# Kernel tuning notes

Hardware: AMD Instinct MI355X
Metric: run time of the kernel (lower is better)

Reference implementation:

```python
import math
import jax, jax.numpy as jnp
import numpy as np

B, P, L = 32, 128, 64
DIN, TE, H, NH, NL = 16, 64, 512, 8, 2
DH = H // NH
DP = DIN + TE
TAU = 300.0
DELTA = 300.0

_PARAM_SPEC = [
    ("te_scale_w", (1, 1)), ("te_scale_b", (1,)),
    ("te_per_w", (TE - 1, 1)), ("te_per_b", (TE - 1,)),
    ("inp_w", (H, DP)), ("inp_b", (H,)),
    ("wq", (H, H)), ("bq", (H,)), ("wk", (H, H)), ("bk", (H,)),
    ("wv", (H, H)), ("bv", (H,)), ("wo", (H, H)), ("bo", (H,)),
    ("ffn_w1", (H, H)), ("ffn_b1", (H,)), ("ffn_w2", (H, H)), ("ffn_b2", (H,)),
    ("ln1_g", (H,)), ("ln1_b", (H,)), ("ln2_g", (H,)), ("ln2_b", (H,)),
    ("exists_bias", (1, 1, H)),
    ("gwq", (NL, H, H)), ("gbq", (NL, H)), ("gwk", (NL, H, H)), ("gbk", (NL, H)),
    ("gwv", (NL, H, H)), ("gbv", (NL, H)), ("gwo", (NL, H, H)), ("gbo", (NL, H)),
]


def setup_inputs() -> dict:
    key = jax.random.key(0)
    ks = jax.random.split(key, 3 + len(_PARAM_SPEC))
    inp = {
        "x": jax.random.normal(ks[0], (B, P, L, DIN), jnp.float32),
        "tt": jax.random.uniform(ks[1], (B, P, L, 1), jnp.float32),
        "mask": jax.random.randint(ks[2], (B, P, L, 1), 0, 2).astype(jnp.int32),
    }
    for i, (name, shp) in enumerate(_PARAM_SPEC):
        inp[name] = 0.02 * jax.random.normal(ks[3 + i], shp, jnp.float32)
    # LayerNorm affine params: gamma=1, beta=0
    inp["ln1_g"] = jnp.ones((H,), jnp.float32)
    inp["ln1_b"] = jnp.zeros((H,), jnp.float32)
    inp["ln2_g"] = jnp.ones((H,), jnp.float32)
    inp["ln2_b"] = jnp.zeros((H,), jnp.float32)
    return inp


def _layernorm(x, g, b, eps=1e-5):
    m = x.mean(-1, keepdims=True)
    v = ((x - m) ** 2).mean(-1, keepdims=True)
    return (x - m) / jnp.sqrt(v + eps) * g + b


def _time_bias(m):
    idx = jnp.arange(m)
    dist = jnp.abs(idx[:, None] - idx[None, :]).astype(jnp.float32) * DELTA
    return jnp.log(jnp.exp(-dist / TAU) + 1e-12)  # [P, P]


def _pos_encoding(p, d):
    pos = jnp.arange(p, dtype=jnp.float32)[:, None]
    div = jnp.exp(jnp.arange(0, d, 2, dtype=jnp.float32) * (-math.log(10000.0) / d))
    pe = jnp.zeros((p, d), jnp.float32)
    pe = pe.at[:, 0::2].set(jnp.sin(pos * div))
    pe = pe.at[:, 1::2].set(jnp.cos(pos * div))
    return pe


def reference(x, tt, mask,
              te_scale_w, te_scale_b, te_per_w, te_per_b,
              inp_w, inp_b, wq, bq, wk, bk, wv, bv, wo, bo,
              ffn_w1, ffn_b1, ffn_w2, ffn_b2, ln1_g, ln1_b, ln2_g, ln2_b,
              exists_bias, gwq, gbq, gwk, gbk, gwv, gbv, gwo, gbo):
    b, p, l, _ = x.shape
    # --- Learnable time embedding: scale linear + sin(periodic linear), concat ---
    te1 = tt @ te_scale_w.T + te_scale_b                      # [B,P,L,1]
    te2 = jnp.sin(tt @ te_per_w.T + te_per_b)                 # [B,P,L,TE-1]
    pts = jnp.concatenate([x, te1, te2], axis=-1)             # [B,P,L,DP]

    valid = (mask[..., 0] > 0).reshape(b * p, l)              # [N,L] bool
    h = (pts.reshape(b * p, l, DP) @ inp_w.T) + inp_b         # [N,L,H]

    has_any = jnp.any(valid, axis=1)                          # [N]
    key_pad = ~valid
    # Empty patches: unmask position 0 and zero its features
    key_pad = key_pad.at[:, 0].set(key_pad[:, 0] & has_any)
    pos0 = (jnp.arange(l) == 0)[None, :, None]
    h = jnp.where((~has_any)[:, None, None] & pos0, 0.0, h)

    # --- Intra-patch MHA (GAT) ---
    def heads(t, w, bias):
        return ((t @ w.T) + bias).reshape(b * p, l, NH, DH)
    q, k, v = heads(h, wq, bq), heads(h, wk, bk), heads(h, wv, bv)
    sc = jnp.einsum("nqhd,nkhd->nhqk", q, k) / math.sqrt(DH)
    sc = jnp.where(key_pad[:, None, None, :], -1e9, sc)
    z = jnp.einsum("nhqk,nkhd->nqhd", jax.nn.softmax(sc, axis=-1), v)
    z = z.reshape(b * p, l, H) @ wo.T + bo
    h = _layernorm(h + z, ln1_g, ln1_b)
    ffn = jax.nn.relu(h @ ffn_w1.T + ffn_b1) @ ffn_w2.T + ffn_b2
    h = _layernorm(h + ffn, ln2_g, ln2_b)

    # Masked mean pooling -> patch tokens
    w = valid.astype(jnp.float32)[..., None]                  # [N,L,1]
    denom = jnp.clip(w.sum(axis=1), 1.0)
    h = ((h * w).sum(axis=1) / denom).reshape(b, p, H)        # [B,P,H]

    # Exists bias for missing patches + positional encoding
    pexists = has_any.reshape(b, p).astype(jnp.float32)       # [B,P]
    h = h + exists_bias * (1.0 - pexists)[..., None]
    h = h + _pos_encoding(p, H)[None]

    # --- Patch-level time-biased graph attention stack (residual) ---
    tb = _time_bias(p)[None, None]                            # [1,1,P,P]
    kp = (pexists <= 0.0)[:, None, None, :]                   # [B,1,1,P]
    for li in range(NL):
        def gh(t, w, bias):
            return ((t @ w.T) + bias).reshape(b, p, NH, DH)
        q = gh(h, gwq[li], gbq[li])
        k = gh(h, gwk[li], gbk[li])
        v = gh(h, gwv[li], gbv[li])
        att = jnp.einsum("bqhd,bkhd->bhqk", q, k) / math.sqrt(DH) + tb
        att = jnp.where(kp, -1e9, att)
        out = jnp.einsum("bhqk,bkhd->bqhd", jax.nn.softmax(att, axis=-1), v)
        out = out.reshape(b, p, H) @ gwo[li].T + gbo[li]
        out = out * pexists[..., None]
        h = h + out
    return h
```

## Files before the change

### kernel.cpp

```cpp
#include <hip/hip_runtime.h>

#define NTOK 4096
#define CH   512
#define NCHUNK 8

typedef _Float16 f16;
typedef __attribute__((ext_vector_type(8))) _Float16 half8;
typedef __attribute__((ext_vector_type(4))) _Float16 half4;
typedef __attribute__((ext_vector_type(4))) float f32x4;

#define OFF_INPW 0
#define OFF_WQKV (512*128)
#define OFF_WO   (OFF_WQKV + 3*512*512)
#define OFF_W1   (OFF_WO + 512*512)
#define OFF_W2   (OFF_W1 + 512*512)
#define OFF_GW   (OFF_W2 + 512*512)
#define WBF_TOT  (OFF_GW + 8*512*512)

static __device__ __forceinline__ f32x4 mfma16(half8 a, half8 b, f32x4 c){
  return __builtin_amdgcn_mfma_f32_16x16x32_f16(a, b, c, 0, 0, 0);
}

static __device__ __forceinline__ void gld_lds16(const f16* g, f16* l){
  __builtin_amdgcn_global_load_lds(
      (const __attribute__((address_space(1))) void*)g,
      (__attribute__((address_space(3))) void*)l, 16, 0, 0);
}

__global__ __launch_bounds__(256) void conv_weights(
    const float* __restrict__ inpw, const float* __restrict__ wq, const float* __restrict__ wk,
    const float* __restrict__ wv, const float* __restrict__ wo, const float* __restrict__ w1,
    const float* __restrict__ w2, const float* __restrict__ gwq, const float* __restrict__ gwk,
    const float* __restrict__ gwv, const float* __restrict__ gwo, f16* __restrict__ wbf,
    const float* __restrict__ bq, const float* __restrict__ bk, const float* __restrict__ bv,
    const float* __restrict__ gbq, const float* __restrict__ gbk, const float* __restrict__ gbv,
    float* __restrict__ biasb)
{
  int e = blockIdx.x*256 + threadIdx.x;
  int y = blockIdx.y;
  if (y == 0){
    if (e < 512*128){
      int row = e>>7, col = e&127;
      float v = (col < 80) ? inpw[row*80 + col] : 0.f;
      wbf[OFF_INPW + e] = (f16)v;
    }
    return;
  }
  if (y == 15){
    if (e < 1536){
      biasb[e] = (e < 512) ? bq[e] : (e < 1024 ? bk[e-512] : bv[e-1024]);
    } else if (e < 3*1536){
      int idx = e - 1536, li = idx/1536, c = idx - li*1536;
      float v = (c < 512) ? gbq[li*512 + c] : (c < 1024 ? gbk[li*512 + c-512] : gbv[li*512 + c-1024]);
      biasb[e] = v;
    }
    return;
  }
  if (e >= 512*512) return;
  const float* src; int off;
  if (y <= 6){
    const float* tab[6] = {wq, wk, wv, wo, w1, w2};
    src = tab[y-1]; off = OFF_WQKV + (y-1)*512*512;
  } else {
    int idx = y-7; int li = idx>>2, part = idx&3;
    const float* tab[4] = {gwq, gwk, gwv, gwo};
    src = tab[part] + (size_t)li*512*512; off = OFF_GW + idx*512*512;
  }
  wbf[off + e] = (f16)src[e];
}

__global__ __launch_bounds__(256) void build_mask(
    const int* __restrict__ mask, float* __restrict__ mb, float* __restrict__ pex)
{
  int wv = threadIdx.x>>6, lane = threadIdx.x&63;
  int n = blockIdx.x*4 + wv;
  int valid = mask[(size_t)n*64 + lane] > 0;
  unsigned long long ball = __ballot(valid);
  int hasany = (ball != 0ull);
  int masked = (lane == 0) ? (!valid && hasany) : (!valid);
  mb[(size_t)n*64 + lane] = masked ? -1e9f : 0.f;
  if (lane == 0) pex[n] = hasany ? 1.f : 0.f;
}

__global__ __launch_bounds__(256) void pts_build(
    const float* __restrict__ x, const float* __restrict__ tt,
    const float* __restrict__ tsw, const float* __restrict__ tsb,
    const float* __restrict__ tpw, const float* __restrict__ tpb,
    f16* __restrict__ pts, int rowbase)
{
  int e = blockIdx.x*256 + threadIdx.x;
  int r = e>>7, col = e&127;
  size_t grow = (size_t)rowbase + r;
  float v;
  if (col < 16) v = x[grow*16 + col];
  else if (col >= 80) v = 0.f;
  else {
    float t = tt[grow];
    if (col == 16) v = t*tsw[0] + tsb[0];
    else           v = __sinf(t*tpw[col-17] + tpb[col-17]);
  }
  pts[e] = (f16)v;
}

template<int RESID, bool RELU, bool OUTF32, bool ZEMPTY>
__global__ __launch_bounds__(256) void gemm128(
    const f16* __restrict__ A, const f16* __restrict__ W, const float* __restrict__ bias,
    void* __restrict__ Cout, const void* __restrict__ Rsd, const float* __restrict__ pex,
    int K, int lda, int ldc, int nbase)
{
  __shared__ __align__(16) f16 As[128][64];
  __shared__ __align__(16) f16 Bs[128][64];
  const int tid = threadIdx.x;
  const int m0 = blockIdx.x*128, n0 = blockIdx.y*128;
  const int wv = tid>>6, lane = tid&63, l15 = lane&15, quad = lane>>4;
  const int wm = (wv&1)*64, wn = (wv>>1)*64;
  const int srow = lane>>3;
  const int schunk = (lane&7) ^ srow;
  f32x4 acc[4][4] = {};
  for (int kc = 0; kc < K; kc += 64){
    __syncthreads();
    #pragma unroll
    for (int i=0; i<4; i++){
      const int rA = wv*32 + i*8;
      gld_lds16(A + (size_t)(m0 + rA + srow)*lda + kc + schunk*8, &As[rA][0]);
      gld_lds16(W + (size_t)(n0 + rA + srow)*K   + kc + schunk*8, &Bs[rA][0]);
    }
    __syncthreads();
    #pragma unroll
    for (int kk=0; kk<2; kk++){
      half8 av[4], bv8[4];
      #pragma unroll
      for (int t=0; t<4; t++){
        const int ra = wm + t*16 + l15;
        av[t]  = *(const half8*)(&As[ra][(((kk*4 + quad) ^ (ra&7)))*8]);
        const int rb = wn + t*16 + l15;
        bv8[t] = *(const half8*)(&Bs[rb][(((kk*4 + quad) ^ (rb&7)))*8]);
      }
      #pragma unroll
      for (int mt=0; mt<4; mt++)
        #pragma unroll
        for (int nt=0; nt<4; nt++)
          acc[mt][nt] = mfma16(av[mt], bv8[nt], acc[mt][nt]);
    }
  }
  #pragma unroll
  for (int mt=0; mt<4; mt++){
    #pragma unroll
    for (int nt=0; nt<4; nt++){
      #pragma unroll
      for (int i=0; i<4; i++){
        int gr = m0 + wm + mt*16 + quad*4 + i;
        int gc = n0 + wn + nt*16 + l15;
        float v = acc[mt][nt][i] + bias[gc];
        if (RELU) v = fmaxf(v, 0.f);
        if (RESID == 1) v += (float)((const f16*)Rsd)[(size_t)gr*ldc + gc];
        if (ZEMPTY){ if ((gr&63)==0 && pex[nbase + (gr>>6)]==0.f) v = 0.f; }
        if (RESID == 2) v = v*pex[gr] + ((const float*)Rsd)[(size_t)gr*ldc + gc];
        if (OUTF32) ((float*)Cout)[(size_t)gr*ldc + gc] = v;
        else        ((f16*)Cout)[(size_t)gr*ldc + gc] = (f16)v;
      }
    }
  }
}

__global__ __launch_bounds__(128) void attn_patch(
    f16* __restrict__ qkv, const float* __restrict__ maskbias, int nbase)
{
  __shared__ f16 Vt[2][64][72];
  __shared__ f16 Ps[2][64][72];
  __shared__ float mbs[64];
  const int tid = threadIdx.x, wv = tid>>6, lane = tid&63, l15 = lane&15, quad = lane>>4;
  const int n = blockIdx.x, h = blockIdx.y*2 + wv;
  if (tid < 64) mbs[tid] = maskbias[(size_t)(nbase+n)*64 + tid];
  const f16* Vb = qkv + 1024 + h*64;
  for (int i=0; i<64; i++)
    Vt[wv][lane][i] = Vb[((size_t)n*64 + i)*1536 + lane];
  __syncthreads();
  const f16* Qb  = qkv + (size_t)n*64*1536 + h*64;
  const f16* Kbb = Qb + 512;
  f32x4 sacc[4][4] = {};
  #pragma unroll
  for (int kc=0; kc<2; kc++){
    half8 af[4], bf[4];
    #pragma unroll
    for (int t4=0; t4<4; t4++){
      af[t4] = *(const half8*)(Qb  + (size_t)(t4*16 + l15)*1536 + kc*32 + quad*8);
      bf[t4] = *(const half8*)(Kbb + (size_t)(t4*16 + l15)*1536 + kc*32 + quad*8);
    }
    #pragma unroll
    for (int ti=0; ti<4; ti++)
      #pragma unroll
      for (int tj=0; tj<4; tj++)
        sacc[ti][tj] = mfma16(af[ti], bf[tj], sacc[ti][tj]);
  }
  #pragma unroll
  for (int ti=0; ti<4; ti++){
    #pragma unroll
    for (int i=0; i<4; i++){
      float mx = -1e30f;
      #pragma unroll
      for (int tj=0; tj<4; tj++){
        float sv = sacc[ti][tj][i]*0.125f + mbs[tj*16 + l15];
        sacc[ti][tj][i] = sv;
        mx = fmaxf(mx, sv);
      }
      #pragma unroll
      for (int off=1; off<16; off<<=1) mx = fmaxf(mx, __shfl_xor(mx, off, 64));
      float sum = 0.f;
      #pragma unroll
      for (int tj=0; tj<4; tj++){
        float pv = __expf(sacc[ti][tj][i] - mx);
        sacc[ti][tj][i] = pv; sum += pv;
      }
      #pragma unroll
      for (int off=1; off<16; off<<=1) sum += __shfl_xor(sum, off, 64);
      float inv = 1.f/sum;
      int q = ti*16 + quad*4 + i;
      #pragma unroll
      for (int tj=0; tj<4; tj++)
        Ps[wv][q][tj*16 + l15] = (f16)(sacc[ti][tj][i]*inv);
    }
  }
  __syncthreads();
  f32x4 zacc[4][4] = {};
  #pragma unroll
  for (int kc=0; kc<2; kc++){
    half8 va[4], pb[4];
    #pragma unroll
    for (int t4=0; t4<4; t4++){
      va[t4] = *(const half8*)(&Vt[wv][t4*16 + l15][kc*32 + quad*8]);
      pb[t4] = *(const half8*)(&Ps[wv][t4*16 + l15][kc*32 + quad*8]);
    }
    #pragma unroll
    for (int ti2=0; ti2<4; ti2++)
      #pragma unroll
      for (int tj=0; tj<4; tj++)
        zacc[ti2][tj] = mfma16(va[ti2], pb[tj], zacc[ti2][tj]);
  }
  __syncthreads();
  #pragma unroll
  for (int ti2=0; ti2<4; ti2++)
    #pragma unroll
    for (int tj=0; tj<4; tj++){
      int q = tj*16 + l15, d0 = ti2*16 + quad*4;
      half4 pk;
      #pragma unroll
      for (int i=0; i<4; i++) pk[i] = (f16)zacc[ti2][tj][i];
      *(half4*)(&Vt[wv][q][d0]) = pk;
    }
  __syncthreads();
  #pragma unroll
  for (int i=0; i<8; i++){
    int q = i*8 + (lane>>3), d0 = (lane&7)*8;
    *(uint4*)(qkv + ((size_t)n*64 + q)*1536 + h*64 + d0) = *(const uint4*)(&Vt[wv][q][d0]);
  }
}

__global__ __launch_bounds__(256) void ln_rows(
    const f16* __restrict__ X, f16* __restrict__ Y,
    const float* __restrict__ g, const float* __restrict__ b)
{
  int wv = threadIdx.x>>6, lane = threadIdx.x&63;
  size_t row = (size_t)blockIdx.x*4 + wv;
  half8 raw = *(const half8*)(X + row*512 + lane*8);
  float xv[8];
  #pragma unroll
  for (int j=0; j<8; j++) xv[j] = (float)raw[j];
  float s = 0.f;
  #pragma unroll
  for (int j=0; j<8; j++) s += xv[j];
  #pragma unroll
  for (int off=1; off<64; off<<=1) s += __shfl_xor(s, off, 64);
  float mean = s*(1.f/512.f);
  float vs = 0.f;
  #pragma unroll
  for (int j=0; j<8; j++){ float d = xv[j]-mean; vs += d*d; }
  #pragma unroll
  for (int off=1; off<64; off<<=1) vs += __shfl_xor(vs, off, 64);
  float rstd = rsqrtf(vs*(1.f/512.f) + 1e-5f);
  half8 o;
  #pragma unroll
  for (int j=0; j<8; j++){
    int c = lane*8 + j;
    o[j] = (f16)((xv[j]-mean)*rstd*g[c] + b[c]);
  }
  *(half8*)(Y + row*512 + lane*8) = o;
}

__global__ __launch_bounds__(256) void pool_ln2(
    const f16* __restrict__ X, const int* __restrict__ mask,
    const float* __restrict__ g, const float* __restrict__ b, const float* __restrict__ eb,
    float* __restrict__ out, int nbase)
{
  __shared__ float mArr[64], rArr[64], vArr[64];
  const int tid = threadIdx.x, wv = tid>>6, lane = tid&63;
  const int n = blockIdx.x, ng = nbase + n, p = ng & 127;
  for (int j=0; j<16; j++){
    int l = wv*16 + j;
    half8 raw = *(const half8*)(X + ((size_t)n*64 + l)*512 + lane*8);
    float s=0.f, ss=0.f;
    #pragma unroll
    for (int jj=0; jj<8; jj++){ float f = (float)raw[jj]; s += f; ss += f*f; }
    #pragma unroll
    for (int off=1; off<64; off<<=1){ s += __shfl_xor(s, off, 64); ss += __shfl_xor(ss, off, 64); }
    if (lane == 0){
      float m = s*(1.f/512.f);
      mArr[l] = m; rArr[l] = rsqrtf(ss*(1.f/512.f) - m*m + 1e-5f);
    }
  }
  if (tid < 64) vArr[tid] = (mask[(size_t)ng*64 + tid] > 0) ? 1.f : 0.f;
  __syncthreads();
  float cnt = 0.f;
  #pragma unroll
  for (int l=0; l<64; l++) cnt += vArr[l];
  float denom = fmaxf(cnt, 1.f);
  float pexv = cnt > 0.f ? 1.f : 0.f;
  float a0=0.f, a1=0.f;
  for (int l=0; l<64; l++){
    float wgt = vArr[l], m = mArr[l], rs = rArr[l];
    float x0 = (float)X[((size_t)n*64+l)*512 + tid];
    float x1 = (float)X[((size_t)n*64+l)*512 + tid + 256];
    a0 += wgt*(x0-m)*rs; a1 += wgt*(x1-m)*rs;
  }
  #pragma unroll
  for (int k=0; k<2; k++){
    int c = tid + k*256;
    float acc = k ? a1 : a0;
    float fr = __expf(-(float)(c & ~1) * (9.210340371976184f/512.f));
    float ang = (float)p * fr;
    float pe = (c & 1) ? cosf(ang) : sinf(ang);
    float o = (g[c]*acc + b[c]*cnt)/denom + eb[c]*(1.f - pexv) + pe;
    out[(size_t)ng*512 + c] = o;
  }
}

__global__ __launch_bounds__(256) void cvt_f32_f16(const float* __restrict__ s, f16* __restrict__ d){
  int i = blockIdx.x*256 + threadIdx.x;
  d[i] = (f16)s[i];
}

__global__ __launch_bounds__(256) void attn_graph(
    f16* __restrict__ qkv, const float* __restrict__ pexists)
{
  __shared__ f16 Vt[64][136];
  __shared__ f16 Ps[4][32][136];
  __shared__ float pxs[128];
  const int tid = threadIdx.x, wv = tid>>6, lane = tid&63, l15 = lane&15, quad = lane>>4;
  const int b = blockIdx.x, h = blockIdx.y;
  if (tid < 128) pxs[tid] = pexists[b*128 + tid];
  const f16* Vb = qkv + 1024 + h*64;
  for (int i=0; i<32; i++){
    int e = tid + i*256, k = e>>6, d = e&63;
    Vt[d][k] = Vb[((size_t)b*128 + k)*1536 + d];
  }
  __syncthreads();
  const f16* Qb = qkv + h*64;
  const f16* Kb = qkv + 512 + h*64;
  const int qb = wv*32;
  f32x4 sacc[2][8] = {};
  #pragma unroll
  for (int kc=0; kc<2; kc++){
    half8 af[2], bf[8];
    #pragma unroll
    for (int ti=0; ti<2; ti++)
      af[ti] = *(const half8*)(Qb + ((size_t)b*128 + qb + ti*16 + l15)*1536 + kc*32 + quad*8);
    #pragma unroll
    for (int tj=0; tj<8; tj++)
      bf[tj] = *(const half8*)(Kb + ((size_t)b*128 + tj*16 + l15)*1536 + kc*32 + quad*8);
    #pragma unroll
    for (int ti=0; ti<2; ti++)
      #pragma unroll
      for (int tj=0; tj<8; tj++)
        sacc[ti][tj] = mfma16(af[ti], bf[tj], sacc[ti][tj]);
  }
  #pragma unroll
  for (int ti=0; ti<2; ti++){
    #pragma unroll
    for (int i=0; i<4; i++){
      int q = qb + ti*16 + quad*4 + i;
      float mx = -1e30f;
      #pragma unroll
      for (int tj=0; tj<8; tj++){
        int col = tj*16 + l15;
        int dd = q - col; if (dd < 0) dd = -dd;
        float tb = __logf(__expf(-(float)dd) + 1e-12f);
        float sv = sacc[ti][tj][i]*0.125f + tb + (pxs[col] > 0.f ? 0.f : -1e9f);
        sacc[ti][tj][i] = sv;
        mx = fmaxf(mx, sv);
      }
      #pragma unroll
      for (int off=1; off<16; off<<=1) mx = fmaxf(mx, __shfl_xor(mx, off, 64));
      float sum = 0.f;
      #pragma unroll
      for (int tj=0; tj<8; tj++){
        float pv = __expf(sacc[ti][tj][i] - mx);
        sacc[ti][tj][i] = pv; sum += pv;
      }
      #pragma unroll
      for (int off=1; off<16; off<<=1) sum += __shfl_xor(sum, off, 64);
      float inv = 1.f/sum;
      int ql = ti*16 + quad*4 + i;
      #pragma unroll
      for (int tj=0; tj<8; tj++)
        Ps[wv][ql][tj*16 + l15] = (f16)(sacc[ti][tj][i]*inv);
    }
  }
  __syncthreads();
  f32x4 zacc[4][2] = {};
  #pragma unroll
  for (int kc=0; kc<4; kc++){
    half8 va[4], pb[2];
    #pragma unroll
    for (int ti2=0; ti2<4; ti2++)
      va[ti2] = *(const half8*)(&Vt[ti2*16 + l15][kc*32 + quad*8]);
    #pragma unroll
    for (int tjq=0; tjq<2; tjq++)
      pb[tjq] = *(const half8*)(&Ps[wv][tjq*16 + l15][kc*32 + quad*8]);
    #pragma unroll
    for (int ti2=0; ti2<4; ti2++)
      #pragma unroll
      for (int tjq=0; tjq<2; tjq++)
        zacc[ti2][tjq] = mfma16(va[ti2], pb[tjq], zacc[ti2][tjq]);
  }
  __syncthreads();
  #pragma unroll
  for (int ti2=0; ti2<4; ti2++)
    #pragma unroll
    for (int tjq=0; tjq<2; tjq++){
      int ql = tjq*16 + l15, d0 = ti2*16 + quad*4;
      half4 pk;
      #pragma unroll
      for (int i=0; i<4; i++) pk[i] = (f16)zacc[ti2][tjq][i];
      *(half4*)(&Ps[wv][ql][d0]) = pk;
    }
  __syncthreads();
  {
    int q = tid>>1, hf = tid&1;
    const f16* src = &Ps[q>>5][q&31][hf*32];
    #pragma unroll
    for (int j=0; j<4; j++)
      *(uint4*)(qkv + ((size_t)b*128 + q)*1536 + h*64 + hf*32 + j*8) = *(const uint4*)(src + j*8);
  }
}

extern "C" void kernel_launch(void* const* d_in, const int* in_sizes, int n_in,
                              void* d_out, int out_size, void* d_ws, size_t ws_size,
                              hipStream_t stream)
{
  (void)in_sizes; (void)n_in; (void)out_size; (void)ws_size;
  const float* x    = (const float*)d_in[0];
  const float* tt   = (const float*)d_in[1];
  const int*   mask = (const int*)  d_in[2];
  const float* tsw  = (const float*)d_in[3];
  const float* tsb  = (const float*)d_in[4];
  const float* tpw  = (const float*)d_in[5];
  const float* tpb  = (const float*)d_in[6];
  const float* inpw = (const float*)d_in[7];
  const float* inpb = (const float*)d_in[8];
  const float* wq   = (const float*)d_in[9];
  const float* bq   = (const float*)d_in[10];
  const float* wk   = (const float*)d_in[11];
  const float* bk   = (const float*)d_in[12];
  const float* wv   = (const float*)d_in[13];
  const float* bv   = (const float*)d_in[14];
  const float* wo   = (const float*)d_in[15];
  const float* bo   = (const float*)d_in[16];
  const float* w1   = (const float*)d_in[17];
  const float* b1   = (const float*)d_in[18];
  const float* w2   = (const float*)d_in[19];
  const float* b2   = (const float*)d_in[20];
  const float* ln1g = (const float*)d_in[21];
  const float* ln1b = (const float*)d_in[22];
  const float* ln2g = (const float*)d_in[23];
  const float* ln2b = (const float*)d_in[24];
  const float* eb   = (const float*)d_in[25];
  const float* gwq  = (const float*)d_in[26];
  const float* gbq  = (const float*)d_in[27];
  const float* gwk  = (const float*)d_in[28];
  const float* gbk  = (const float*)d_in[29];
  const float* gwv  = (const float*)d_in[30];
  const float* gbv  = (const float*)d_in[31];
  const float* gwo  = (const float*)d_in[32];
  const float* gbo  = (const float*)d_in[33];
  float* out = (float*)d_out;

  char* wp = (char*)d_ws;
  auto alloc = [&](size_t bytes)->char*{
    char* p = wp; wp += (bytes + 255) & ~(size_t)255; return p;
  };
  f16*   wbf   = (f16*)  alloc((size_t)WBF_TOT*2);
  float* mb    = (float*)alloc((size_t)NTOK*64*4);
  float* pex   = (float*)alloc((size_t)NTOK*4);
  float* biasb = (float*)alloc((size_t)3*1536*4);
  f16*   ptsb  = (f16*)  alloc((size_t)CH*64*128*2);
  f16*   bufA  = (f16*)  alloc((size_t)CH*64*512*2);
  f16*   bufB  = (f16*)  alloc((size_t)CH*64*512*2);
  f16*   bufC  = (f16*)  alloc((size_t)CH*64*512*2);
  f16*   qkv   = (f16*)  alloc((size_t)CH*64*1536*2);

  conv_weights<<<dim3(1024,16),256,0,stream>>>(inpw,wq,wk,wv,wo,w1,w2,gwq,gwk,gwv,gwo,wbf,
                                               bq,bk,bv,gbq,gbk,gbv,biasb);
  build_mask<<<NTOK/4,256,0,stream>>>(mask, mb, pex);

  const int MB = CH*64/128;
  for (int ch=0; ch<NCHUNK; ch++){
    int nbase = ch*CH;
    int rowbase = nbase*64;
    pts_build<<<CH*64*128/256,256,0,stream>>>(x,tt,tsw,tsb,tpw,tpb,ptsb,rowbase);
    gemm128<0,false,false,true ><<<dim3(MB,4),256,0,stream>>>(ptsb, wbf+OFF_INPW, inpb, bufA, nullptr, pex, 128, 128, 512, nbase);
    gemm128<0,false,false,false><<<dim3(MB,12),256,0,stream>>>(bufA, wbf+OFF_WQKV, biasb, qkv, nullptr, nullptr, 512, 512, 1536, 0);
    attn_patch<<<dim3(CH,4),128,0,stream>>>(qkv, mb, nbase);
    gemm128<1,false,false,false><<<dim3(MB,4),256,0,stream>>>(qkv, wbf+OFF_WO, bo, bufA, bufA, nullptr, 512, 1536, 512, 0);
    ln_rows<<<CH*64/4,256,0,stream>>>(bufA, bufB, ln1g, ln1b);
    gemm128<0,true ,false,false><<<dim3(MB,4),256,0,stream>>>(bufB, wbf+OFF_W1, b1, bufC, nullptr, nullptr, 512, 512, 512, 0);
    gemm128<1,false,false,false><<<dim3(MB,4),256,0,stream>>>(bufC, wbf+OFF_W2, b2, bufB, bufB, nullptr, 512, 512, 512, 0);
    pool_ln2<<<CH,256,0,stream>>>(bufB, mask, ln2g, ln2b, eb, out, nbase);
  }

  f16* hbf  = bufA;
  f16* qkvg = bufB;
  for (int li=0; li<2; li++){
    cvt_f32_f16<<<NTOK*512/256,256,0,stream>>>(out, hbf);
    gemm128<0,false,false,false><<<dim3(32,12),256,0,stream>>>(hbf, wbf+OFF_GW + (size_t)li*4*512*512, biasb + 1536*(1+li), qkvg, nullptr, nullptr, 512, 512, 1536, 0);
    attn_graph<<<dim3(32,8),256,0,stream>>>(qkvg, pex);
    gemm128<2,false,true ,false><<<dim3(32,4),256,0,stream>>>(qkvg, wbf+OFF_GW + (size_t)(li*4+3)*512*512, gbo+li*512, out, out, pex, 512, 1536, 512, 0);
  }
}
```

Baseline: 2.466 ms.

## Add 256x256 pipelined GEMM kernel for large per-chunk projections

Adds a gemm256 kernel with 512 threads (8 waves), 256x256 output tiles, double-buffered LDS filled through global_load_lds with XOR swizzle, and a split-phase schedule that interleaves quarter-tile loads with MFMA groups between barriers, plus setprio and an XCD-aware block swizzle. The QKV, Wo, FFN1 and FFN2 GEMMs in the patch encoder now use it in place of the 128x128 kernel. The aim is more data reuse per loaded tile and better overlap of global loads with MFMA work. The cost is large register use (128 accumulator floats per thread) and larger LDS, which may limit occupancy; the grids are also smaller (64x2 blocks for N=512).

```diff
diff --git a/kernel.cpp b/kernel.cpp
--- a/kernel.cpp
+++ b/kernel.cpp
@@ -26,6 +26,12 @@
       (const __attribute__((address_space(1))) void*)g,
       (__attribute__((address_space(3))) void*)l, 16, 0, 0);
 }
+
+#define FULL_BARRIER() do { \
+    asm volatile("" ::: "memory"); \
+    __builtin_amdgcn_s_barrier(); \
+    __builtin_amdgcn_sched_barrier(0); \
+  } while(0)
 
 __global__ __launch_bounds__(256) void conv_weights(
     const float* __restrict__ inpw, const float* __restrict__ wq, const float* __restrict__ wk,
@@ -158,6 +164,126 @@
         if (RESID == 2) v = v*pex[gr] + ((const float*)Rsd)[(size_t)gr*ldc + gc];
         if (OUTF32) ((float*)Cout)[(size_t)gr*ldc + gc] = v;
         else        ((f16*)Cout)[(size_t)gr*ldc + gc] = (f16)v;
+      }
+    }
+  }
+}
+
+template<int RESID, bool RELU>
+__global__ __launch_bounds__(512,2) void gemm256(
+    const f16* __restrict__ A, const f16* __restrict__ W, const float* __restrict__ bias,
+    f16* __restrict__ Cout, const f16* __restrict__ Rsd,
+    int K, int lda, int ldc)
+{
+  __shared__ __align__(16) f16 As[2*2*128*64];
+  __shared__ __align__(16) f16 Bs[2*2*128*64];
+
+  const int tid = threadIdx.x;
+  const int wv = tid>>6, lane = tid&63, l15 = lane&15, quad = lane>>4;
+  const int wm = wv>>2;
+  const int wn = wv&3;
+
+  const int gx = gridDim.x, gy = gridDim.y;
+  int nwg = gx*gy;
+  int orig = blockIdx.x*gy + blockIdx.y;
+  int qq = nwg>>3;
+  int swz = (orig&7)*qq + (orig>>3);
+  const int m0 = (swz/gy)*256, n0 = (swz%gy)*256;
+
+  const int NT = K>>6;
+
+  auto stage_half = [&](int t, int hf){
+    int tc = t < NT ? t : NT-1;
+    int kc = tc<<6;
+    int b  = t & 1;
+    #pragma unroll
+    for (int i=0;i<2;i++){
+      int idx = wv*2+i;
+      int row = idx*8 + (lane>>3);
+      int col = kc + (((lane&7) ^ (lane>>3))<<3);
+      if (hf < 2)
+        gld_lds16(A + (size_t)(m0 + hf*128 + row)*lda + col,
+                  As + b*16384 + hf*8192 + idx*512);
+      else
+        gld_lds16(W + (size_t)(n0 + (hf-2)*128 + row)*K + col,
+                  Bs + b*16384 + (hf-2)*8192 + idx*512);
+    }
+  };
+  auto ldsA = [&](int b, int mt, int kk)->half8{
+    int r = mt*16 + l15;
+    int g = kk*4 + quad;
+    return *(const half8*)(As + b*16384 + wm*8192 + r*64 + ((g ^ (r&7))<<3));
+  };
+  auto ldsB = [&](int b, int nt, int kk)->half8{
+    int r = (wn&1)*64 + nt*16 + l15;
+    int g = kk*4 + quad;
+    return *(const half8*)(Bs + b*16384 + (wn>>1)*8192 + r*64 + ((g ^ (r&7))<<3));
+  };
+
+  half8 a[8], b0[4], b1[4];
+  f32x4 acc[8][4] = {};
+  auto mm8 = [&](int mb, half8* bq, int nb){
+    __builtin_amdgcn_s_setprio(1);
+    #pragma unroll
+    for (int m=0;m<4;m++)
+      #pragma unroll
+      for (int n=0;n<2;n++)
+        #pragma unroll
+        for (int k=0;k<2;k++)
+          acc[mb+m][nb+n] = mfma16(a[m*2+k], bq[n*2+k], acc[mb+m][nb+n]);
+    __builtin_amdgcn_s_setprio(0);
+  };
+
+  stage_half(0,0); stage_half(0,1); stage_half(0,2); stage_half(0,3);
+  stage_half(1,0);
+  asm volatile("s_waitcnt vmcnt(2)" ::: "memory");
+  FULL_BARRIER();
+
+  for (int t = 0; t < NT; t += 2){
+    #pragma unroll
+    for (int hv = 0; hv < 2; hv++){
+      const int bf = hv;
+      const int ts = t + 1 + hv;
+      #pragma unroll
+      for (int m=0;m<4;m++){ a[m*2]=ldsA(bf,m,0); a[m*2+1]=ldsA(bf,m,1); }
+      #pragma unroll
+      for (int n=0;n<2;n++){ b0[n*2]=ldsB(bf,n,0); b0[n*2+1]=ldsB(bf,n,1); }
+      stage_half(ts, 1);
+      FULL_BARRIER();
+      mm8(0, b0, 0);
+      FULL_BARRIER();
+      #pragma unroll
+      for (int n=0;n<2;n++){ b1[n*2]=ldsB(bf,n+2,0); b1[n*2+1]=ldsB(bf,n+2,1); }
+      stage_half(ts, 2);
+      FULL_BARRIER();
+      mm8(0, b1, 2);
+      FULL_BARRIER();
+      #pragma unroll
+      for (int m=0;m<4;m++){ a[m*2]=ldsA(bf,m+4,0); a[m*2+1]=ldsA(bf,m+4,1); }
+      stage_half(ts, 3);
+      FULL_BARRIER();
+      mm8(4, b1, 2);
+      FULL_BARRIER();
+      stage_half(ts+1, 0);
+      asm volatile("s_waitcnt vmcnt(2)" ::: "memory");
+      FULL_BARRIER();
+      mm8(4, b0, 0);
+      FULL_BARRIER();
+    }
+  }
+
+  #pragma unroll
+  for (int mt=0; mt<8; mt++){
+    #pragma unroll
+    for (int nt=0; nt<4; nt++){
+      #pragma unroll
+      for (int i=0; i<4; i++){
+        int gr = m0 + wm*128 + mt*16 + quad*4 + i;
+        int gc = n0 + wn*64  + nt*16 + l15;
+        float v = acc[mt][nt][i] + bias[gc];
+        if (RELU) v = fmaxf(v, 0.f);
+        if (RESID == 1) v += (float)Rsd[(size_t)gr*ldc + gc];
+        Cout[(size_t)gr*ldc + gc] = (f16)v;
       }
     }
   }
@@ -502,18 +628,19 @@
                                                bq,bk,bv,gbq,gbk,gbv,biasb);
   build_mask<<<NTOK/4,256,0,stream>>>(mask, mb, pex);
 
-  const int MB = CH*64/128;
+  const int MB  = CH*64/128;
+  const int MB2 = CH*64/256;
   for (int ch=0; ch<NCHUNK; ch++){
     int nbase = ch*CH;
     int rowbase = nbase*64;
     pts_build<<<CH*64*128/256,256,0,stream>>>(x,tt,tsw,tsb,tpw,tpb,ptsb,rowbase);
     gemm128<0,false,false,true ><<<dim3(MB,4),256,0,stream>>>(ptsb, wbf+OFF_INPW, inpb, bufA, nullptr, pex, 128, 128, 512, nbase);
-    gemm128<0,false,false,false><<<dim3(MB,12),256,0,stream>>>(bufA, wbf+OFF_WQKV, biasb, qkv, nullptr, nullptr, 512, 512, 1536, 0);
+    gemm256<0,false><<<dim3(MB2,6),512,0,stream>>>(bufA, wbf+OFF_WQKV, biasb, qkv, nullptr, 512, 512, 1536);
     attn_patch<<<dim3(CH,4),128,0,stream>>>(qkv, mb, nbase);
-    gemm128<1,false,false,false><<<dim3(MB,4),256,0,stream>>>(qkv, wbf+OFF_WO, bo, bufA, bufA, nullptr, 512, 1536, 512, 0);
+    gemm256<1,false><<<dim3(MB2,2),512,0,stream>>>(qkv, wbf+OFF_WO, bo, bufA, bufA, 512, 1536, 512);
     ln_rows<<<CH*64/4,256,0,stream>>>(bufA, bufB, ln1g, ln1b);
-    gemm128<0,true ,false,false><<<dim3(MB,4),256,0,stream>>>(bufB, wbf+OFF_W1, b1, bufC, nullptr, nullptr, 512, 512, 512, 0);
-    gemm128<1,false,false,false><<<dim3(MB,4),256,0,stream>>>(bufC, wbf+OFF_W2, b2, bufB, bufB, nullptr, 512, 512, 512, 0);
+    gemm256<0,true ><<<dim3(MB2,2),512,0,stream>>>(bufB, wbf+OFF_W1, b1, bufC, nullptr, 512, 512, 512);
+    gemm256<1,false><<<dim3(MB2,2),512,0,stream>>>(bufC, wbf+OFF_W2, b2, bufB, bufB, 512, 512, 512);
     pool_ln2<<<CH,256,0,stream>>>(bufB, mask, ln2g, ln2b, eb, out, nbase);
   }
 
```

After: 2.358 ms. 4.4% less time.

## Fuse per-patch QKV, attention, Wo, LN1, FFN, LN2 and pooling into one kernel

Applied to the files above, without the earlier changes.

Replaces the per-chunk chain of QKV GEMM, patch attention, Wo GEMM, LayerNorm, two FFN GEMMs and pool/LN2 with a single patch_block kernel. Each block handles one patch of 64 tokens and keeps intermediates in shared memory, so the large qkv and FFN activation buffers are never written to or read from global memory. Chunk size grows from 512 to 2048 patches, which cuts launches further. In exchange, every block re-reads the full 512x512 weight matrices straight from global memory without LDS tiling, and the kernel has heavy register and LDS use that may lower occupancy.

```diff
diff --git a/kernel.cpp b/kernel.cpp
--- a/kernel.cpp
+++ b/kernel.cpp
@@ -1,8 +1,8 @@
 #include <hip/hip_runtime.h>
 
 #define NTOK 4096
-#define CH   512
-#define NCHUNK 8
+#define CH   2048
+#define NCHUNK 2
 
 typedef _Float16 f16;
 typedef __attribute__((ext_vector_type(8))) _Float16 half8;
@@ -163,176 +163,341 @@
   }
 }
 
-__global__ __launch_bounds__(128) void attn_patch(
-    f16* __restrict__ qkv, const float* __restrict__ maskbias, int nbase)
+__global__ __launch_bounds__(256) void patch_block(
+    const f16* __restrict__ h0g, const f16* __restrict__ wbf, const float* __restrict__ biasb,
+    const float* __restrict__ bo, const float* __restrict__ b1f, const float* __restrict__ b2f,
+    const float* __restrict__ g1, const float* __restrict__ be1,
+    const float* __restrict__ g2, const float* __restrict__ be2,
+    const float* __restrict__ eb, const float* __restrict__ mb,
+    const int* __restrict__ mask, float* __restrict__ out, int nbase)
 {
-  __shared__ f16 Vt[2][64][72];
-  __shared__ f16 Ps[2][64][72];
-  __shared__ float mbs[64];
+  __shared__ __align__(16) f16 Z[64*520];
+  __shared__ __align__(16) f16 SC[4*2*64*72];
+  __shared__ float stS[64][4], stQ[64][4];
+  __shared__ float mbs[64], vArr[64];
+
   const int tid = threadIdx.x, wv = tid>>6, lane = tid&63, l15 = lane&15, quad = lane>>4;
-  const int n = blockIdx.x, h = blockIdx.y*2 + wv;
-  if (tid < 64) mbs[tid] = maskbias[(size_t)(nbase+n)*64 + tid];
-  const f16* Vb = qkv + 1024 + h*64;
-  for (int i=0; i<64; i++)
-    Vt[wv][lane][i] = Vb[((size_t)n*64 + i)*1536 + lane];
+  const int n = blockIdx.x, ng = nbase + n;
+  const size_t rbase = (size_t)n*64;
+
+  if (tid < 64){
+    mbs[tid]  = mb[(size_t)ng*64 + tid];
+    vArr[tid] = (mask[(size_t)ng*64 + tid] > 0) ? 1.f : 0.f;
+  }
   __syncthreads();
-  const f16* Qb  = qkv + (size_t)n*64*1536 + h*64;
-  const f16* Kbb = Qb + 512;
-  f32x4 sacc[4][4] = {};
-  #pragma unroll
-  for (int kc=0; kc<2; kc++){
-    half8 af[4], bf[4];
-    #pragma unroll
-    for (int t4=0; t4<4; t4++){
-      af[t4] = *(const half8*)(Qb  + (size_t)(t4*16 + l15)*1536 + kc*32 + quad*8);
-      bf[t4] = *(const half8*)(Kbb + (size_t)(t4*16 + l15)*1536 + kc*32 + quad*8);
-    }
-    #pragma unroll
-    for (int ti=0; ti<4; ti++)
-      #pragma unroll
-      for (int tj=0; tj<4; tj++)
-        sacc[ti][tj] = mfma16(af[ti], bf[tj], sacc[ti][tj]);
-  }
-  #pragma unroll
-  for (int ti=0; ti<4; ti++){
-    #pragma unroll
-    for (int i=0; i<4; i++){
-      float mx = -1e30f;
-      #pragma unroll
-      for (int tj=0; tj<4; tj++){
-        float sv = sacc[ti][tj][i]*0.125f + mbs[tj*16 + l15];
-        sacc[ti][tj][i] = sv;
-        mx = fmaxf(mx, sv);
-      }
-      #pragma unroll
-      for (int off=1; off<16; off<<=1) mx = fmaxf(mx, __shfl_xor(mx, off, 64));
-      float sum = 0.f;
-      #pragma unroll
-      for (int tj=0; tj<4; tj++){
-        float pv = __expf(sacc[ti][tj][i] - mx);
-        sacc[ti][tj][i] = pv; sum += pv;
-      }
-      #pragma unroll
-      for (int off=1; off<16; off<<=1) sum += __shfl_xor(sum, off, 64);
-      float inv = 1.f/sum;
-      int q = ti*16 + quad*4 + i;
-      #pragma unroll
-      for (int tj=0; tj<4; tj++)
-        Ps[wv][q][tj*16 + l15] = (f16)(sacc[ti][tj][i]*inv);
+
+  f16* Qb = SC + wv*(2*64*72);
+  f16* Kb = Qb + 64*72;
+  const f16* Wq = wbf + OFF_WQKV;
+
+  #pragma unroll 1
+  for (int hr=0; hr<2; hr++){
+    const int h = wv*2 + hr;
+    {
+      f32x4 qa[4][4] = {}, ka[4][4] = {};
+      #pragma unroll 4
+      for (int ks=0; ks<16; ks++){
+        half8 a[4], bq_[4], bk_[4];
+        #pragma unroll
+        for (int mt=0; mt<4; mt++)
+          a[mt] = *(const half8*)(h0g + (rbase + mt*16 + l15)*512 + ks*32 + quad*8);
+        #pragma unroll
+        for (int nt=0; nt<4; nt++){
+          bq_[nt] = *(const half8*)(Wq + (size_t)(h*64 + nt*16 + l15)*512 + ks*32 + quad*8);
+          bk_[nt] = *(const half8*)(Wq + (size_t)(512 + h*64 + nt*16 + l15)*512 + ks*32 + quad*8);
+        }
+        #pragma unroll
+        for (int mt=0; mt<4; mt++)
+          #pragma unroll
+          for (int nt=0; nt<4; nt++){
+            qa[mt][nt] = mfma16(a[mt], bq_[nt], qa[mt][nt]);
+            ka[mt][nt] = mfma16(a[mt], bk_[nt], ka[mt][nt]);
+          }
+      }
+      #pragma unroll
+      for (int nt=0; nt<4; nt++){
+        float vbq = biasb[h*64 + nt*16 + l15];
+        float vbk = biasb[512 + h*64 + nt*16 + l15];
+        #pragma unroll
+        for (int mt=0; mt<4; mt++)
+          #pragma unroll
+          for (int i=0; i<4; i++){
+            int r = mt*16 + quad*4 + i, c = nt*16 + l15;
+            Qb[r*72 + c] = (f16)(qa[mt][nt][i] + vbq);
+            Kb[r*72 + c] = (f16)(ka[mt][nt][i] + vbk);
+          }
+      }
+    }
+    __syncthreads();
+    {
+      f32x4 sacc[4][4] = {};
+      #pragma unroll
+      for (int kc=0; kc<2; kc++){
+        half8 af[4], bf[4];
+        #pragma unroll
+        for (int t=0; t<4; t++){
+          af[t] = *(const half8*)(Qb + (t*16 + l15)*72 + kc*32 + quad*8);
+          bf[t] = *(const half8*)(Kb + (t*16 + l15)*72 + kc*32 + quad*8);
+        }
+        #pragma unroll
+        for (int ti=0; ti<4; ti++)
+          #pragma unroll
+          for (int tj=0; tj<4; tj++)
+            sacc[ti][tj] = mfma16(af[ti], bf[tj], sacc[ti][tj]);
+      }
+      #pragma unroll
+      for (int ti=0; ti<4; ti++){
+        #pragma unroll
+        for (int i=0; i<4; i++){
+          float mx = -1e30f;
+          #pragma unroll
+          for (int tj=0; tj<4; tj++){
+            float sv = sacc[ti][tj][i]*0.125f + mbs[tj*16 + l15];
+            sacc[ti][tj][i] = sv;
+            mx = fmaxf(mx, sv);
+          }
+          #pragma unroll
+          for (int off=1; off<16; off<<=1) mx = fmaxf(mx, __shfl_xor(mx, off, 64));
+          float sum = 0.f;
+          #pragma unroll
+          for (int tj=0; tj<4; tj++){
+            float pv = __expf(sacc[ti][tj][i] - mx);
+            sacc[ti][tj][i] = pv; sum += pv;
+          }
+          #pragma unroll
+          for (int off=1; off<16; off<<=1) sum += __shfl_xor(sum, off, 64);
+          float inv = 1.f/sum;
+          int q = ti*16 + quad*4 + i;
+          #pragma unroll
+          for (int tj=0; tj<4; tj++)
+            Qb[q*72 + tj*16 + l15] = (f16)(sacc[ti][tj][i]*inv);
+        }
+      }
+    }
+    {
+      f32x4 va4[4][4] = {};
+      #pragma unroll 4
+      for (int ks=0; ks<16; ks++){
+        half8 a[4], bv_[4];
+        #pragma unroll
+        for (int mt=0; mt<4; mt++)
+          a[mt] = *(const half8*)(h0g + (rbase + mt*16 + l15)*512 + ks*32 + quad*8);
+        #pragma unroll
+        for (int nt=0; nt<4; nt++)
+          bv_[nt] = *(const half8*)(Wq + (size_t)(1024 + h*64 + nt*16 + l15)*512 + ks*32 + quad*8);
+        #pragma unroll
+        for (int mt=0; mt<4; mt++)
+          #pragma unroll
+          for (int nt=0; nt<4; nt++)
+            va4[mt][nt] = mfma16(a[mt], bv_[nt], va4[mt][nt]);
+      }
+      #pragma unroll
+      for (int nt=0; nt<4; nt++){
+        float vb = biasb[1024 + h*64 + nt*16 + l15];
+        #pragma unroll
+        for (int mt=0; mt<4; mt++)
+          #pragma unroll
+          for (int i=0; i<4; i++){
+            int tok = mt*16 + quad*4 + i, d = nt*16 + l15;
+            Kb[d*72 + tok] = (f16)(va4[mt][nt][i] + vb);
+          }
+      }
+    }
+    __syncthreads();
+    {
+      f32x4 zacc[4][4] = {};
+      #pragma unroll
+      for (int kc=0; kc<2; kc++){
+        half8 vvf[4], ppf[4];
+        #pragma unroll
+        for (int t=0; t<4; t++){
+          vvf[t] = *(const half8*)(Kb + (t*16 + l15)*72 + kc*32 + quad*8);
+          ppf[t] = *(const half8*)(Qb + (t*16 + l15)*72 + kc*32 + quad*8);
+        }
+        #pragma unroll
+        for (int ti=0; ti<4; ti++)
+          #pragma unroll
+          for (int tj=0; tj<4; tj++)
+            zacc[ti][tj] = mfma16(vvf[ti], ppf[tj], zacc[ti][tj]);
+      }
+      #pragma unroll
+      for (int ti=0; ti<4; ti++)
+        #pragma unroll
+        for (int tj=0; tj<4; tj++){
+          int q = tj*16 + l15, d0 = ti*16 + quad*4;
+          half4 pk;
+          #pragma unroll
+          for (int i=0; i<4; i++) pk[i] = (f16)zacc[ti][tj][i];
+          *(half4*)(Z + q*520 + h*64 + d0) = pk;
+        }
+    }
+    __syncthreads();
+  }
+
+  auto gemmNK = [&](const f16* Ap, const f16* Wg, f32x4 (&acc)[4][8]){
+    #pragma unroll 2
+    for (int ks=0; ks<16; ks++){
+      half8 a[4], b[8];
+      #pragma unroll
+      for (int mt=0; mt<4; mt++)
+        a[mt] = *(const half8*)(Ap + (mt*16 + l15)*520 + ks*32 + quad*8);
+      #pragma unroll
+      for (int nt=0; nt<8; nt++)
+        b[nt] = *(const half8*)(Wg + (size_t)(wv*128 + nt*16 + l15)*512 + ks*32 + quad*8);
+      #pragma unroll
+      for (int mt=0; mt<4; mt++)
+        #pragma unroll
+        for (int nt=0; nt<8; nt++)
+          acc[mt][nt] = mfma16(a[mt], b[nt], acc[mt][nt]);
+    }
+  };
+
+  {
+    f32x4 oa[4][8] = {};
+    gemmNK(Z, wbf + OFF_WO, oa);
+    #pragma unroll
+    for (int nt=0; nt<8; nt++){
+      int c = wv*128 + nt*16 + l15;
+      float bv = bo[c];
+      #pragma unroll
+      for (int mt=0; mt<4; mt++)
+        #pragma unroll
+        for (int i=0; i<4; i++){
+          int r = mt*16 + quad*4 + i;
+          oa[mt][nt][i] += bv + (float)h0g[(rbase + r)*512 + c];
+        }
+    }
+    #pragma unroll
+    for (int mt=0; mt<4; mt++)
+      #pragma unroll
+      for (int i=0; i<4; i++){
+        float s = 0.f, sq = 0.f;
+        #pragma unroll
+        for (int nt=0; nt<8; nt++){ float v = oa[mt][nt][i]; s += v; sq += v*v; }
+        #pragma unroll
+        for (int off=1; off<16; off<<=1){ s += __shfl_xor(s, off, 64); sq += __shfl_xor(sq, off, 64); }
+        if (l15 == 0){
+          int r = mt*16 + quad*4 + i;
+          stS[r][wv] = s; stQ[r][wv] = sq;
+        }
+      }
+    __syncthreads();
+    float m_[4][4], rs_[4][4];
+    #pragma unroll
+    for (int mt=0; mt<4; mt++)
+      #pragma unroll
+      for (int i=0; i<4; i++){
+        int r = mt*16 + quad*4 + i;
+        float ts = stS[r][0] + stS[r][1] + stS[r][2] + stS[r][3];
+        float tq = stQ[r][0] + stQ[r][1] + stQ[r][2] + stQ[r][3];
+        float m = ts*(1.f/512.f);
+        m_[mt][i] = m;
+        rs_[mt][i] = rsqrtf(tq*(1.f/512.f) - m*m + 1e-5f);
+      }
+    #pragma unroll
+    for (int nt=0; nt<8; nt++){
+      int c = wv*128 + nt*16 + l15;
+      float g1c = g1[c], be1c = be1[c];
+      #pragma unroll
+      for (int mt=0; mt<4; mt++)
+        #pragma unroll
+        for (int i=0; i<4; i++){
+          int r = mt*16 + quad*4 + i;
+          float hl = (oa[mt][nt][i] - m_[mt][i])*rs_[mt][i]*g1c + be1c;
+          Z[r*520 + c] = (f16)hl;
+        }
     }
   }
   __syncthreads();
-  f32x4 zacc[4][4] = {};
-  #pragma unroll
-  for (int kc=0; kc<2; kc++){
-    half8 va[4], pb[4];
-    #pragma unroll
-    for (int t4=0; t4<4; t4++){
-      va[t4] = *(const half8*)(&Vt[wv][t4*16 + l15][kc*32 + quad*8]);
-      pb[t4] = *(const half8*)(&Ps[wv][t4*16 + l15][kc*32 + quad*8]);
-    }
-    #pragma unroll
-    for (int ti2=0; ti2<4; ti2++)
-      #pragma unroll
-      for (int tj=0; tj<4; tj++)
-        zacc[ti2][tj] = mfma16(va[ti2], pb[tj], zacc[ti2][tj]);
+
+  {
+    f32x4 fa[4][8] = {};
+    gemmNK(Z, wbf + OFF_W1, fa);
+    #pragma unroll
+    for (int nt=0; nt<8; nt++){
+      int c = wv*128 + nt*16 + l15;
+      float bv = b1f[c];
+      #pragma unroll
+      for (int mt=0; mt<4; mt++)
+        #pragma unroll
+        for (int i=0; i<4; i++){
+          int r = mt*16 + quad*4 + i;
+          SC[r*520 + c] = (f16)fmaxf(fa[mt][nt][i] + bv, 0.f);
+        }
+    }
   }
   __syncthreads();
-  #pragma unroll
-  for (int ti2=0; ti2<4; ti2++)
-    #pragma unroll
-    for (int tj=0; tj<4; tj++){
-      int q = tj*16 + l15, d0 = ti2*16 + quad*4;
-      half4 pk;
-      #pragma unroll
-      for (int i=0; i<4; i++) pk[i] = (f16)zacc[ti2][tj][i];
-      *(half4*)(&Vt[wv][q][d0]) = pk;
-    }
-  __syncthreads();
-  #pragma unroll
-  for (int i=0; i<8; i++){
-    int q = i*8 + (lane>>3), d0 = (lane&7)*8;
-    *(uint4*)(qkv + ((size_t)n*64 + q)*1536 + h*64 + d0) = *(const uint4*)(&Vt[wv][q][d0]);
-  }
-}
-
-__global__ __launch_bounds__(256) void ln_rows(
-    const f16* __restrict__ X, f16* __restrict__ Y,
-    const float* __restrict__ g, const float* __restrict__ b)
-{
-  int wv = threadIdx.x>>6, lane = threadIdx.x&63;
-  size_t row = (size_t)blockIdx.x*4 + wv;
-  half8 raw = *(const half8*)(X + row*512 + lane*8);
-  float xv[8];
-  #pragma unroll
-  for (int j=0; j<8; j++) xv[j] = (float)raw[j];
-  float s = 0.f;
-  #pragma unroll
-  for (int j=0; j<8; j++) s += xv[j];
-  #pragma unroll
-  for (int off=1; off<64; off<<=1) s += __shfl_xor(s, off, 64);
-  float mean = s*(1.f/512.f);
-  float vs = 0.f;
-  #pragma unroll
-  for (int j=0; j<8; j++){ float d = xv[j]-mean; vs += d*d; }
-  #pragma unroll
-  for (int off=1; off<64; off<<=1) vs += __shfl_xor(vs, off, 64);
-  float rstd = rsqrtf(vs*(1.f/512.f) + 1e-5f);
-  half8 o;
-  #pragma unroll
-  for (int j=0; j<8; j++){
-    int c = lane*8 + j;
-    o[j] = (f16)((xv[j]-mean)*rstd*g[c] + b[c]);
-  }
-  *(half8*)(Y + row*512 + lane*8) = o;
-}
-
-__global__ __launch_bounds__(256) void pool_ln2(
-    const f16* __restrict__ X, const int* __restrict__ mask,
-    const float* __restrict__ g, const float* __restrict__ b, const float* __restrict__ eb,
-    float* __restrict__ out, int nbase)
-{
-  __shared__ float mArr[64], rArr[64], vArr[64];
-  const int tid = threadIdx.x, wv = tid>>6, lane = tid&63;
-  const int n = blockIdx.x, ng = nbase + n, p = ng & 127;
-  for (int j=0; j<16; j++){
-    int l = wv*16 + j;
-    half8 raw = *(const half8*)(X + ((size_t)n*64 + l)*512 + lane*8);
-    float s=0.f, ss=0.f;
-    #pragma unroll
-    for (int jj=0; jj<8; jj++){ float f = (float)raw[jj]; s += f; ss += f*f; }
-    #pragma unroll
-    for (int off=1; off<64; off<<=1){ s += __shfl_xor(s, off, 64); ss += __shfl_xor(ss, off, 64); }
-    if (lane == 0){
-      float m = s*(1.f/512.f);
-      mArr[l] = m; rArr[l] = rsqrtf(ss*(1.f/512.f) - m*m + 1e-5f);
-    }
-  }
-  if (tid < 64) vArr[tid] = (mask[(size_t)ng*64 + tid] > 0) ? 1.f : 0.f;
-  __syncthreads();
-  float cnt = 0.f;
-  #pragma unroll
-  for (int l=0; l<64; l++) cnt += vArr[l];
-  float denom = fmaxf(cnt, 1.f);
-  float pexv = cnt > 0.f ? 1.f : 0.f;
-  float a0=0.f, a1=0.f;
-  for (int l=0; l<64; l++){
-    float wgt = vArr[l], m = mArr[l], rs = rArr[l];
-    float x0 = (float)X[((size_t)n*64+l)*512 + tid];
-    float x1 = (float)X[((size_t)n*64+l)*512 + tid + 256];
-    a0 += wgt*(x0-m)*rs; a1 += wgt*(x1-m)*rs;
-  }
-  #pragma unroll
-  for (int k=0; k<2; k++){
-    int c = tid + k*256;
-    float acc = k ? a1 : a0;
-    float fr = __expf(-(float)(c & ~1) * (9.210340371976184f/512.f));
-    float ang = (float)p * fr;
-    float pe = (c & 1) ? cosf(ang) : sinf(ang);
-    float o = (g[c]*acc + b[c]*cnt)/denom + eb[c]*(1.f - pexv) + pe;
-    out[(size_t)ng*512 + c] = o;
-  }
-}
+
+  {
+    f32x4 xa[4][8] = {};
+    gemmNK(SC, wbf + OFF_W2, xa);
+    #pragma unroll
+    for (int nt=0; nt<8; nt++){
+      int c = wv*128 + nt*16 + l15;
+      float bv = b2f[c];
+      #pragma unroll
+      for (int mt=0; mt<4; mt++)
+        #pragma unroll
+        for (int i=0; i<4; i++){
+          int r = mt*16 + quad*4 + i;
+          xa[mt][nt][i] += bv + (float)Z[r*520 + c];
+        }
+    }
+    #pragma unroll
+    for (int mt=0; mt<4; mt++)
+      #pragma unroll
+      for (int i=0; i<4; i++){
+        float s = 0.f, sq = 0.f;
+        #pragma unroll
+        for (int nt=0; nt<8; nt++){ float v = xa[mt][nt][i]; s += v; sq += v*v; }
+        #pragma unroll
+        for (int off=1; off<16; off<<=1){ s += __shfl_xor(s, off, 64); sq += __shfl_xor(sq, off, 64); }
+        if (l15 == 0){
+          int r = mt*16 + quad*4 + i;
+          stS[r][wv] = s; stQ[r][wv] = sq;
+        }
+      }
+    __syncthreads();
+    float m_[4][4], rs_[4][4], wA[4][4];
+    #pragma unroll
+    for (int mt=0; mt<4; mt++)
+      #pragma unroll
+      for (int i=0; i<4; i++){
+        int r = mt*16 + quad*4 + i;
+        float ts = stS[r][0] + stS[r][1] + stS[r][2] + stS[r][3];
+        float tq = stQ[r][0] + stQ[r][1] + stQ[r][2] + stQ[r][3];
+        float m = ts*(1.f/512.f);
+        m_[mt][i] = m;
+        rs_[mt][i] = rsqrtf(tq*(1.f/512.f) - m*m + 1e-5f);
+        wA[mt][i] = vArr[r];
+      }
+    float cnt = 0.f;
+    #pragma unroll
+    for (int l=0; l<64; l++) cnt += vArr[l];
+    float denom = fmaxf(cnt, 1.f);
+    float pexv = cnt > 0.f ? 1.f : 0.f;
+    int pidx = ng & 127;
+    #pragma unroll
+    for (int nt=0; nt<8; nt++){
+      int c = wv*128 + nt*16 + l15;
+      float p = 0.f;
+      #pragma unroll
+      for (int mt=0; mt<4; mt++)
+        #pragma unroll
+        for (int i=0; i<4; i++)
+          p += wA[mt][i]*(xa[mt][nt][i] - m_[mt][i])*rs_[mt][i];
+      p += __shfl_xor(p, 16, 64);
+      p += __shfl_xor(p, 32, 64);
+      if (quad == 0){
+        float fr = __expf(-(float)(c & ~1) * (9.210340371976184f/512.f));
+        float ang = (float)pidx * fr;
+        float pe = (c & 1) ? cosf(ang) : sinf(ang);
+        out[(size_t)ng*512 + c] = (g2[c]*p + be2[c]*cnt)/denom + eb[c]*(1.f - pexv) + pe;
+      }
+    }
+  }
+}
+
 
 __global__ __launch_bounds__(256) void cvt_f32_f16(const float* __restrict__ s, f16* __restrict__ d){
   int i = blockIdx.x*256 + threadIdx.x;
@@ -494,31 +659,22 @@
   float* biasb = (float*)alloc((size_t)3*1536*4);
   f16*   ptsb  = (f16*)  alloc((size_t)CH*64*128*2);
   f16*   bufA  = (f16*)  alloc((size_t)CH*64*512*2);
-  f16*   bufB  = (f16*)  alloc((size_t)CH*64*512*2);
-  f16*   bufC  = (f16*)  alloc((size_t)CH*64*512*2);
-  f16*   qkv   = (f16*)  alloc((size_t)CH*64*1536*2);
+  f16*   hbf   = (f16*)  alloc((size_t)NTOK*512*2);
+  f16*   qkvg  = (f16*)  alloc((size_t)NTOK*1536*2);
 
   conv_weights<<<dim3(1024,16),256,0,stream>>>(inpw,wq,wk,wv,wo,w1,w2,gwq,gwk,gwv,gwo,wbf,
                                                bq,bk,bv,gbq,gbk,gbv,biasb);
   build_mask<<<NTOK/4,256,0,stream>>>(mask, mb, pex);
 
-  const int MB = CH*64/128;
   for (int ch=0; ch<NCHUNK; ch++){
     int nbase = ch*CH;
     int rowbase = nbase*64;
     pts_build<<<CH*64*128/256,256,0,stream>>>(x,tt,tsw,tsb,tpw,tpb,ptsb,rowbase);
-    gemm128<0,false,false,true ><<<dim3(MB,4),256,0,stream>>>(ptsb, wbf+OFF_INPW, inpb, bufA, nullptr, pex, 128, 128, 512, nbase);
-    gemm128<0,false,false,false><<<dim3(MB,12),256,0,stream>>>(bufA, wbf+OFF_WQKV, biasb, qkv, nullptr, nullptr, 512, 512, 1536, 0);
-    attn_patch<<<dim3(CH,4),128,0,stream>>>(qkv, mb, nbase);
-    gemm128<1,false,false,false><<<dim3(MB,4),256,0,stream>>>(qkv, wbf+OFF_WO, bo, bufA, bufA, nullptr, 512, 1536, 512, 0);
-    ln_rows<<<CH*64/4,256,0,stream>>>(bufA, bufB, ln1g, ln1b);
-    gemm128<0,true ,false,false><<<dim3(MB,4),256,0,stream>>>(bufB, wbf+OFF_W1, b1, bufC, nullptr, nullptr, 512, 512, 512, 0);
-    gemm128<1,false,false,false><<<dim3(MB,4),256,0,stream>>>(bufC, wbf+OFF_W2, b2, bufB, bufB, nullptr, 512, 512, 512, 0);
-    pool_ln2<<<CH,256,0,stream>>>(bufB, mask, ln2g, ln2b, eb, out, nbase);
-  }
-
-  f16* hbf  = bufA;
-  f16* qkvg = bufB;
+    gemm128<0,false,false,true ><<<dim3(CH*64/128,4),256,0,stream>>>(ptsb, wbf+OFF_INPW, inpb, bufA, nullptr, pex, 128, 128, 512, nbase);
+    patch_block<<<CH,256,0,stream>>>(bufA, wbf, biasb, bo, b1, b2,
+                                     ln1g, ln1b, ln2g, ln2b, eb, mb, mask, out, nbase);
+  }
+
   for (int li=0; li<2; li++){
     cvt_f32_f16<<<NTOK*512/256,256,0,stream>>>(out, hbf);
     gemm128<0,false,false,false><<<dim3(32,12),256,0,stream>>>(hbf, wbf+OFF_GW + (size_t)li*4*512*512, biasb + 1536*(1+li), qkvg, nullptr, nullptr, 512, 512, 1536, 0);
```

Measured after the change: 3.029 ms. 22.9% more time.
